# Kernel tuning notes

Measured on AMD Instinct MI355X. Metric: run time of the kernel, lower is better.

## Reference

```python
import jax, jax.numpy as jnp
import numpy as np

NUM_HEADS = 4  # nn.MultiheadAttention(num_heads=4)


def setup_inputs() -> dict:
    key = jax.random.key(0)
    ks = jax.random.split(key, 9)
    E, D, B, S = 16, 128, 8, 512
    H2 = D // 2
    s = 0.05
    return {
        "lstm_features": jax.random.normal(ks[0], (B, S, D), dtype=jnp.float32),
        "Wqkv": jax.random.normal(ks[1], (E, 3 * D, D), dtype=jnp.float32) * s,
        "bqkv": jax.random.normal(ks[2], (E, 3 * D), dtype=jnp.float32) * s,
        "Wo": jax.random.normal(ks[3], (E, D, D), dtype=jnp.float32) * s,
        "bo": jax.random.normal(ks[4], (E, D), dtype=jnp.float32) * s,
        "W1": jax.random.normal(ks[5], (E, H2, D), dtype=jnp.float32) * s,
        "b1": jax.random.normal(ks[6], (E, H2), dtype=jnp.float32) * s,
        "W2": jax.random.normal(ks[7], (E, 1, H2), dtype=jnp.float32) * s,
        "b2": jax.random.normal(ks[8], (E, 1), dtype=jnp.float32) * s,
    }


def reference(lstm_features, Wqkv, bqkv, Wo, bo, W1, b1, W2, b2):
    # lstm_features: [B, S, D]; params stacked over E=num_events.
    B, S, D = lstm_features.shape
    E = Wqkv.shape[0]
    H = NUM_HEADS
    Dh = D // H

    # Grouped in-projection for all events at once: [E, B, S, 3D]
    qkv = jnp.einsum("bsd,ekd->ebsk", lstm_features, Wqkv) + bqkv[:, None, None, :]
    q, k, v = jnp.split(qkv, 3, axis=-1)  # each [E, B, S, D]

    def heads(t):  # [E,B,S,D] -> [E,B,H,S,Dh]
        return t.reshape(E, B, S, H, Dh).transpose(0, 1, 3, 2, 4)

    q, k, v = heads(q), heads(k), heads(v)

    scale = 1.0 / jnp.sqrt(jnp.asarray(Dh, dtype=lstm_features.dtype))
    scores = jnp.einsum("ebhqd,ebhkd->ebhqk", q, k) * scale  # [E,B,H,S,S]
    attn = jax.nn.softmax(scores, axis=-1)
    ctx = jnp.einsum("ebhqk,ebhkd->ebhqd", attn, v)  # [E,B,H,S,Dh]
    ctx = ctx.transpose(0, 1, 3, 2, 4).reshape(E, B, S, D)

    attended = jnp.einsum("ebsd,eod->ebso", ctx, Wo) + bo[:, None, None, :]

    # Per-event MLP head: D -> D//2 -> 1 (dropout is identity in eval)
    h = jax.nn.relu(jnp.einsum("ebsd,ehd->ebsh", attended, W1) + b1[:, None, None, :])
    logits = jnp.einsum("ebsh,eoh->ebso", h, W2) + b2[:, None, None, :]  # [E,B,S,1]
    logits = logits[..., 0]  # [E,B,S]

    # torch.stack(..., dim=2) -> [B, S, E]
    return logits.transpose(1, 2, 0)
```

## Files before the change

### kernel.cpp

```cpp
#include <hip/hip_runtime.h>


#define E_ 16
#define B_ 8
#define S_ 512
#define D_ 128
#define H_ 4
#define DH_ 32
#define H2_ 64
#define M_ (B_ * S_)
#define QK_SCALE 0.17677669529663687f

typedef __attribute__((ext_vector_type(4))) short bf16x4;
typedef __attribute__((ext_vector_type(8))) short bf16x8;
typedef __attribute__((ext_vector_type(4))) float f32x4;

__device__ __forceinline__ short f2bf(float f) {
    unsigned u = __builtin_bit_cast(unsigned, f);
    u += 0x7fffu + ((u >> 16) & 1u);
    return (short)(u >> 16);
}

__device__ __forceinline__ bf16x8 cat8(bf16x4 lo, bf16x4 hi) {
    return __builtin_shufflevector(lo, hi, 0, 1, 2, 3, 4, 5, 6, 7);
}

__global__ __launch_bounds__(256) void convert_kernel(
    const float* __restrict__ x, const float* __restrict__ w,
    const float* __restrict__ wo, const float* __restrict__ w1,
    short* __restrict__ xbf, short* __restrict__ wbf,
    short* __restrict__ wobf, short* __restrict__ w1bf)
{
    const int XN  = (M_ * D_) / 8;
    const int WN  = (E_ * 3 * D_ * D_) / 8;
    const int WON = (E_ * D_ * D_) / 8;
    const int W1N = (E_ * H2_ * D_) / 8;
    int idx = blockIdx.x * 256 + threadIdx.x;
    const float* src; short* dst; int off;
    if (idx < XN)                        { src = x;  dst = xbf;  off = idx; }
    else if (idx < XN + WN)              { src = w;  dst = wbf;  off = idx - XN; }
    else if (idx < XN + WN + WON)        { src = wo; dst = wobf; off = idx - XN - WN; }
    else if (idx < XN + WN + WON + W1N)  { src = w1; dst = w1bf; off = idx - XN - WN - WON; }
    else return;
    float4 v0 = *(const float4*)&src[(size_t)off * 8];
    float4 v1 = *(const float4*)&src[(size_t)off * 8 + 4];
    bf16x8 o;
    o[0] = f2bf(v0.x); o[1] = f2bf(v0.y); o[2] = f2bf(v0.z); o[3] = f2bf(v0.w);
    o[4] = f2bf(v1.x); o[5] = f2bf(v1.y); o[6] = f2bf(v1.z); o[7] = f2bf(v1.w);
    *(bf16x8*)&dst[(size_t)off * 8] = o;
}

__global__ __launch_bounds__(256) void qkv_mfma_kernel(
    const short* __restrict__ xbf,
    const short* __restrict__ wbf,
    const float* __restrict__ bqkv,
    short* __restrict__ q, short* __restrict__ k, short* __restrict__ v)
{
    __shared__ __align__(16) char lds[2 * 64 * 136 * 2];
    short (*xs)[136] = (short(*)[136])lds;
    short (*ws)[136] = (short(*)[136])(lds + 64 * 136 * 2);

    const int ct = blockIdx.x;
    const int rt = blockIdx.y;
    const int e  = blockIdx.z;
    const int tid = threadIdx.x;
    const int w    = tid >> 6;
    const int lane = tid & 63;
    const int l15  = lane & 15;
    const int g    = lane >> 4;

    #pragma unroll
    for (int p = 0; p < 4; ++p) {
        int idx = tid + p * 256;
        int row = idx >> 4, c8 = (idx & 15) * 8;
        *(bf16x8*)&xs[row][c8] =
            *(const bf16x8*)&xbf[(size_t)(rt * 64 + row) * 128 + c8];
        *(bf16x8*)&ws[row][c8] =
            *(const bf16x8*)&wbf[((size_t)e * 384 + ct * 64 + row) * 128 + c8];
    }
    __syncthreads();

    const int n0 = (w & 1) * 32;
    const int m0 = (w >> 1) * 32;
    f32x4 acc00 = {0.f,0.f,0.f,0.f}, acc01 = {0.f,0.f,0.f,0.f};
    f32x4 acc10 = {0.f,0.f,0.f,0.f}, acc11 = {0.f,0.f,0.f,0.f};

    #pragma unroll
    for (int kk = 0; kk < 128; kk += 32) {
        bf16x8 A0 = cat8(*(const bf16x4*)&ws[n0      + l15][kk + 4 * g],
                         *(const bf16x4*)&ws[n0      + l15][kk + 16 + 4 * g]);
        bf16x8 A1 = cat8(*(const bf16x4*)&ws[n0 + 16 + l15][kk + 4 * g],
                         *(const bf16x4*)&ws[n0 + 16 + l15][kk + 16 + 4 * g]);
        bf16x8 B0 = cat8(*(const bf16x4*)&xs[m0      + l15][kk + 4 * g],
                         *(const bf16x4*)&xs[m0      + l15][kk + 16 + 4 * g]);
        bf16x8 B1 = cat8(*(const bf16x4*)&xs[m0 + 16 + l15][kk + 4 * g],
                         *(const bf16x4*)&xs[m0 + 16 + l15][kk + 16 + 4 * g]);
        acc00 = __builtin_amdgcn_mfma_f32_16x16x32_bf16(A0, B0, acc00, 0, 0, 0);
        acc01 = __builtin_amdgcn_mfma_f32_16x16x32_bf16(A0, B1, acc01, 0, 0, 0);
        acc10 = __builtin_amdgcn_mfma_f32_16x16x32_bf16(A1, B0, acc10, 0, 0, 0);
        acc11 = __builtin_amdgcn_mfma_f32_16x16x32_bf16(A1, B1, acc11, 0, 0, 0);
    }

    if (ct < 4) {
        short* dst = (ct < 2) ? q : k;
        const float scale = (ct < 2) ? QK_SCALE : 1.0f;
        #define STORE_QK(ACC, NS, MS) {                                          \
            const int jb = ct * 64 + n0 + (NS) * 16 + 4 * g;                     \
            const int d  = jb & 127;                                             \
            const int h  = d >> 5, dh = d & 31;                                  \
            const float b0 = bqkv[e * 384 + jb + 0];                             \
            const float b1 = bqkv[e * 384 + jb + 1];                             \
            const float b2 = bqkv[e * 384 + jb + 2];                             \
            const float b3 = bqkv[e * 384 + jb + 3];                             \
            const int m  = rt * 64 + m0 + (MS) * 16 + l15;                       \
            const int bb = m >> 9, s = m & 511;                                  \
            bf16x4 o;                                                            \
            o[0] = f2bf((ACC[0] + b0) * scale);                                  \
            o[1] = f2bf((ACC[1] + b1) * scale);                                  \
            o[2] = f2bf((ACC[2] + b2) * scale);                                  \
            o[3] = f2bf((ACC[3] + b3) * scale);                                  \
            *(bf16x4*)&dst[((((size_t)e * B_ + bb) * H_ + h) * S_ + s) * DH_ + dh] = o; \
        }
        STORE_QK(acc00, 0, 0); STORE_QK(acc01, 0, 1);
        STORE_QK(acc10, 1, 0); STORE_QK(acc11, 1, 1);
        #undef STORE_QK
    } else {
        __syncthreads();
        float (*rp)[68] = (float(*)[68])lds;
        #define RP(ACC, NS, MS) {                                                \
            const int jl = n0 + (NS) * 16 + 4 * g;                               \
            const int ml = m0 + (MS) * 16 + l15;                                 \
            rp[jl + 0][ml] = ACC[0]; rp[jl + 1][ml] = ACC[1];                    \
            rp[jl + 2][ml] = ACC[2]; rp[jl + 3][ml] = ACC[3];                    \
        }
        RP(acc00, 0, 0); RP(acc01, 0, 1); RP(acc10, 1, 0); RP(acc11, 1, 1);
        #undef RP
        __syncthreads();
        const int bb = (rt * 64) >> 9;
        const int sb = (rt * 64) & 511;
        #pragma unroll
        for (int p = 0; p < 2; ++p) {
            int task = tid + p * 256;
            int jl = task >> 3, sc = (task & 7) * 8;
            const int col = ct * 64 + jl;
            const int d = col & 127, h = d >> 5, dh = d & 31;
            const float bias = bqkv[e * 384 + col];
            bf16x8 o;
            #pragma unroll
            for (int j = 0; j < 8; ++j) o[j] = f2bf(rp[jl][sc + j] + bias);
            *(bf16x8*)&v[((((size_t)e * B_ + bb) * H_ + h) * DH_ + dh) * S_ + sb + sc] = o;
        }
    }
}

__global__ __launch_bounds__(512) void attn_kernel(
    const short* __restrict__ q, const short* __restrict__ k,
    const short* __restrict__ vt, short* __restrict__ ctxbf)
{
    __shared__ alignas(16) short Ks[256][40];
    __shared__ alignas(16) short VTs[32][520];

    const int bh  = blockIdx.x;
    const int e   = blockIdx.y;
    const int tid = threadIdx.x;
    const int w    = tid >> 6;
    const int lane = tid & 63;
    const int l15  = lane & 15;
    const int g    = lane >> 4;

    const size_t base = ((size_t)e * 32 + bh) * (S_ * DH_);
    const short* qg = q  + base;
    const short* kg = k  + base;
    const short* vg = vt + base;

    {
        int d = tid >> 4, c0 = (tid & 15) * 32;
        const uint4* src = (const uint4*)(vg + (size_t)d * S_ + c0);
        uint4* dst = (uint4*)((char*)&VTs[0][0] + (size_t)d * 1040 + c0 * 2);
        dst[0] = src[0]; dst[1] = src[1]; dst[2] = src[2]; dst[3] = src[3];
    }
    {
        int row = tid >> 1, ch = (tid & 1) * 16;
        const uint4* src = (const uint4*)(kg + (size_t)row * DH_ + ch);
        uint4* dst = (uint4*)((char*)&Ks[0][0] + (size_t)row * 80 + ch * 2);
        dst[0] = src[0]; dst[1] = src[1];
    }
    bf16x8 bq[4];
    int qrow[4];
    #pragma unroll
    for (int qf = 0; qf < 4; ++qf) {
        qrow[qf] = w * 64 + qf * 16 + l15;
        bf16x4 lo = *(const bf16x4*)(qg + (size_t)qrow[qf] * DH_ + 4 * g);
        bf16x4 hi = *(const bf16x4*)(qg + (size_t)qrow[qf] * DH_ + 16 + 4 * g);
        bq[qf] = cat8(lo, hi);
    }
    __syncthreads();

    f32x4 acc0[4] = {}, acc1[4] = {};
    float lsum[4] = {0.f, 0.f, 0.f, 0.f};

    for (int half = 0; half < 2; ++half) {
        for (int kt = 0; kt < 8; ++kt) {
            bf16x8 ka[2];
            #pragma unroll
            for (int tt = 0; tt < 2; ++tt) {
                const int row_l = (kt * 2 + tt) * 16 + l15;
                const char* kp = (const char*)&Ks[0][0] + (size_t)row_l * 80 + g * 8;
                ka[tt] = cat8(*(const bf16x4*)kp, *(const bf16x4*)(kp + 32));
            }
            const int keyb = half * 256 + kt * 32;
            const char* vp = (const char*)&VTs[0][0] + (size_t)l15 * 1040 + (keyb + 4 * g) * 2;
            bf16x8 va0 = cat8(*(const bf16x4*)vp, *(const bf16x4*)(vp + 32));
            const char* vp1 = vp + 16 * 1040;
            bf16x8 va1 = cat8(*(const bf16x4*)vp1, *(const bf16x4*)(vp1 + 32));

            #pragma unroll
            for (int qf = 0; qf < 4; ++qf) {
                f32x4 z = {0.f, 0.f, 0.f, 0.f};
                f32x4 s0 = __builtin_amdgcn_mfma_f32_16x16x32_bf16(ka[0], bq[qf], z, 0, 0, 0);
                f32x4 s1 = __builtin_amdgcn_mfma_f32_16x16x32_bf16(ka[1], bq[qf], z, 0, 0, 0);
                float p0 = __expf(s0[0]), p1 = __expf(s0[1]);
                float p2 = __expf(s0[2]), p3 = __expf(s0[3]);
                float p4 = __expf(s1[0]), p5 = __expf(s1[1]);
                float p6 = __expf(s1[2]), p7 = __expf(s1[3]);
                lsum[qf] += ((p0 + p1) + (p2 + p3)) + ((p4 + p5) + (p6 + p7));
                bf16x8 pf;
                pf[0] = f2bf(p0); pf[1] = f2bf(p1); pf[2] = f2bf(p2); pf[3] = f2bf(p3);
                pf[4] = f2bf(p4); pf[5] = f2bf(p5); pf[6] = f2bf(p6); pf[7] = f2bf(p7);
                acc0[qf] = __builtin_amdgcn_mfma_f32_16x16x32_bf16(va0, pf, acc0[qf], 0, 0, 0);
                acc1[qf] = __builtin_amdgcn_mfma_f32_16x16x32_bf16(va1, pf, acc1[qf], 0, 0, 0);
            }
        }
        if (half == 0) {
            __syncthreads();
            int row = tid >> 1, ch = (tid & 1) * 16;
            const uint4* src = (const uint4*)(kg + (size_t)(256 + row) * DH_ + ch);
            uint4* dst = (uint4*)((char*)&Ks[0][0] + (size_t)row * 80 + ch * 2);
            dst[0] = src[0]; dst[1] = src[1];
            __syncthreads();
        }
    }

    const int b = bh >> 2, h = bh & 3;
    #pragma unroll
    for (int qf = 0; qf < 4; ++qf) {
        float ls = lsum[qf];
        ls += __shfl_xor(ls, 16);
        ls += __shfl_xor(ls, 32);
        const float inv = 1.0f / ls;
        short* cg = ctxbf + (((size_t)(e * B_ + b) * S_ + qrow[qf]) * D_ + h * DH_);
        bf16x4 o0, o1;
        #pragma unroll
        for (int r = 0; r < 4; ++r) {
            o0[r] = f2bf(acc0[qf][r] * inv);
            o1[r] = f2bf(acc1[qf][r] * inv);
        }
        *(bf16x4*)&cg[4 * g]      = o0;
        *(bf16x4*)&cg[16 + 4 * g] = o1;
    }
}

__global__ __launch_bounds__(256) void head_mfma_kernel(
    const short* __restrict__ ctxbf,
    const short* __restrict__ wobf,
    const float* __restrict__ bo,
    const short* __restrict__ w1bf,
    const float* __restrict__ b1,
    const float* __restrict__ W2,
    const float* __restrict__ b2,
    float* __restrict__ out)
{
    __shared__ alignas(16) short Wos[128][136];
    __shared__ alignas(16) short cts[64][136];

    const int mt  = blockIdx.x;
    const int e   = blockIdx.y;
    const int tid = threadIdx.x;
    const int w    = tid >> 6;
    const int lane = tid & 63;
    const int l15  = lane & 15;
    const int g    = lane >> 4;

    #pragma unroll
    for (int p = 0; p < 8; ++p) {
        int idx = tid + p * 256;
        int row = idx >> 4, c8 = (idx & 15) * 8;
        *(bf16x8*)&Wos[row][c8] =
            *(const bf16x8*)&wobf[((size_t)e * 128 + row) * 128 + c8];
    }
    #pragma unroll
    for (int p = 0; p < 4; ++p) {
        int idx = tid + p * 256;
        int row = idx >> 4, c8 = (idx & 15) * 8;
        *(bf16x8*)&cts[row][c8] =
            *(const bf16x8*)&ctxbf[((size_t)e * M_ + mt * 64 + row) * 128 + c8];
    }
    __syncthreads();

    f32x4 accA[8] = {};
    #pragma unroll
    for (int kk = 0; kk < 128; kk += 32) {
        bf16x8 a = cat8(*(const bf16x4*)&cts[w * 16 + l15][kk + 4 * g],
                        *(const bf16x4*)&cts[w * 16 + l15][kk + 16 + 4 * g]);
        #pragma unroll
        for (int t = 0; t < 8; ++t) {
            bf16x8 bfr = cat8(*(const bf16x4*)&Wos[t * 16 + l15][kk + 4 * g],
                              *(const bf16x4*)&Wos[t * 16 + l15][kk + 16 + 4 * g]);
            accA[t] = __builtin_amdgcn_mfma_f32_16x16x32_bf16(a, bfr, accA[t], 0, 0, 0);
        }
    }
    __syncthreads();

    #pragma unroll
    for (int p = 0; p < 4; ++p) {
        int idx = tid + p * 256;
        int row = idx >> 4, c8 = (idx & 15) * 8;
        *(bf16x8*)&Wos[row][c8] =
            *(const bf16x8*)&w1bf[((size_t)e * 64 + row) * 128 + c8];
    }
    #pragma unroll
    for (int t = 0; t < 8; ++t) {
        const float bov = bo[e * 128 + t * 16 + l15];
        #pragma unroll
        for (int r = 0; r < 4; ++r)
            cts[w * 16 + 4 * g + r][t * 16 + l15] = f2bf(accA[t][r] + bov);
    }
    __syncthreads();

    f32x4 accB[4] = {};
    #pragma unroll
    for (int kk = 0; kk < 128; kk += 32) {
        bf16x8 a = cat8(*(const bf16x4*)&cts[w * 16 + l15][kk + 4 * g],
                        *(const bf16x4*)&cts[w * 16 + l15][kk + 16 + 4 * g]);
        #pragma unroll
        for (int t = 0; t < 4; ++t) {
            bf16x8 bfr = cat8(*(const bf16x4*)&Wos[t * 16 + l15][kk + 4 * g],
                              *(const bf16x4*)&Wos[t * 16 + l15][kk + 16 + 4 * g]);
            accB[t] = __builtin_amdgcn_mfma_f32_16x16x32_bf16(a, bfr, accB[t], 0, 0, 0);
        }
    }

    float b1v[4], w2v[4];
    #pragma unroll
    for (int t = 0; t < 4; ++t) {
        b1v[t] = b1[e * 64 + t * 16 + l15];
        w2v[t] = W2[e * 64 + t * 16 + l15];
    }
    const float b2v = b2[e];
    #pragma unroll
    for (int r = 0; r < 4; ++r) {
        float s = 0.f;
        #pragma unroll
        for (int t = 0; t < 4; ++t)
            s += fmaxf(accB[t][r] + b1v[t], 0.f) * w2v[t];
        s += __shfl_xor(s, 1);
        s += __shfl_xor(s, 2);
        s += __shfl_xor(s, 4);
        s += __shfl_xor(s, 8);
        if (l15 == 0) {
            const int m = mt * 64 + w * 16 + 4 * g + r;
            const int bb = m >> 9, ss = m & 511;
            out[((size_t)(bb * S_ + ss)) * E_ + e] = s + b2v;
        }
    }
}

extern "C" void kernel_launch(void* const* d_in, const int* in_sizes, int n_in,
                              void* d_out, int out_size, void* d_ws, size_t ws_size,
                              hipStream_t stream) {
    const float* x    = (const float*)d_in[0];
    const float* Wqkv = (const float*)d_in[1];
    const float* bqkv = (const float*)d_in[2];
    const float* Wo   = (const float*)d_in[3];
    const float* bo   = (const float*)d_in[4];
    const float* W1   = (const float*)d_in[5];
    const float* b1   = (const float*)d_in[6];
    const float* W2   = (const float*)d_in[7];
    const float* b2   = (const float*)d_in[8];
    float* out = (float*)d_out;

    const size_t SZ = (size_t)E_ * B_ * H_ * S_ * DH_;
    short* qb    = (short*)d_ws;
    short* kb    = qb + SZ;
    short* vtb   = kb + SZ;
    short* ctxbf = vtb + SZ;
    short* xbf   = ctxbf + SZ;
    short* wbf   = xbf + (size_t)M_ * D_;
    short* wobf  = wbf + (size_t)E_ * 3 * D_ * D_;
    short* w1bf  = wobf + (size_t)E_ * D_ * D_;

    convert_kernel<<<dim3(832), 256, 0, stream>>>(x, Wqkv, Wo, W1, xbf, wbf, wobf, w1bf);
    qkv_mfma_kernel<<<dim3(6, 64, 16), 256, 0, stream>>>(xbf, wbf, bqkv, qb, kb, vtb);
    attn_kernel<<<dim3(32, 16), 512, 0, stream>>>(qb, kb, vtb, ctxbf);
    head_mfma_kernel<<<dim3(64, 16), 256, 0, stream>>>(ctxbf, wobf, bo, w1bf, b1, W2, b2, out);
}
```

Measured before the change: 79.41 us.

## Fuse fp32-to-bf16 conversion into GEMM loads and use exp2 softmax

Removes the separate conversion kernel by having the QKV and head GEMM kernels load fp32 inputs and weights directly and pack them to bf16 while staging into LDS. This saves one kernel launch and a write-then-read round trip through the bf16 workspace. It also folds log2(e) into the Q scale so the softmax can use the hardware exp2 instruction, switches to the library bf16 conversion, and partially unrolls the attention key loop. The cost is that weights are now read and converted redundantly by many blocks, and twice as many bytes are loaded per tile.

New measurement: 85.32 us. 7.4% more time.

```diff
diff --git a/kernel.cpp b/kernel.cpp
--- a/kernel.cpp
+++ b/kernel.cpp
@@ -1,4 +1,5 @@
 #include <hip/hip_runtime.h>
+#include <hip/hip_bf16.h>
 
 
 #define E_ 16
@@ -9,50 +10,29 @@
 #define DH_ 32
 #define H2_ 64
 #define M_ (B_ * S_)
-#define QK_SCALE 0.17677669529663687f
+#define QK_SCALE_L2E 0.25503472437616588f
 
 typedef __attribute__((ext_vector_type(4))) short bf16x4;
 typedef __attribute__((ext_vector_type(8))) short bf16x8;
 typedef __attribute__((ext_vector_type(4))) float f32x4;
 
-__device__ __forceinline__ short f2bf(float f) {
-    unsigned u = __builtin_bit_cast(unsigned, f);
-    u += 0x7fffu + ((u >> 16) & 1u);
-    return (short)(u >> 16);
+__device__ __forceinline__ short f2b(float f) {
+    return __builtin_bit_cast(short, __float2bfloat16(f));
+}
+
+__device__ __forceinline__ bf16x4 pack4(float4 v) {
+    bf16x4 o;
+    o[0] = f2b(v.x); o[1] = f2b(v.y); o[2] = f2b(v.z); o[3] = f2b(v.w);
+    return o;
 }
 
 __device__ __forceinline__ bf16x8 cat8(bf16x4 lo, bf16x4 hi) {
     return __builtin_shufflevector(lo, hi, 0, 1, 2, 3, 4, 5, 6, 7);
 }
 
-__global__ __launch_bounds__(256) void convert_kernel(
-    const float* __restrict__ x, const float* __restrict__ w,
-    const float* __restrict__ wo, const float* __restrict__ w1,
-    short* __restrict__ xbf, short* __restrict__ wbf,
-    short* __restrict__ wobf, short* __restrict__ w1bf)
-{
-    const int XN  = (M_ * D_) / 8;
-    const int WN  = (E_ * 3 * D_ * D_) / 8;
-    const int WON = (E_ * D_ * D_) / 8;
-    const int W1N = (E_ * H2_ * D_) / 8;
-    int idx = blockIdx.x * 256 + threadIdx.x;
-    const float* src; short* dst; int off;
-    if (idx < XN)                        { src = x;  dst = xbf;  off = idx; }
-    else if (idx < XN + WN)              { src = w;  dst = wbf;  off = idx - XN; }
-    else if (idx < XN + WN + WON)        { src = wo; dst = wobf; off = idx - XN - WN; }
-    else if (idx < XN + WN + WON + W1N)  { src = w1; dst = w1bf; off = idx - XN - WN - WON; }
-    else return;
-    float4 v0 = *(const float4*)&src[(size_t)off * 8];
-    float4 v1 = *(const float4*)&src[(size_t)off * 8 + 4];
-    bf16x8 o;
-    o[0] = f2bf(v0.x); o[1] = f2bf(v0.y); o[2] = f2bf(v0.z); o[3] = f2bf(v0.w);
-    o[4] = f2bf(v1.x); o[5] = f2bf(v1.y); o[6] = f2bf(v1.z); o[7] = f2bf(v1.w);
-    *(bf16x8*)&dst[(size_t)off * 8] = o;
-}
-
 __global__ __launch_bounds__(256) void qkv_mfma_kernel(
-    const short* __restrict__ xbf,
-    const short* __restrict__ wbf,
+    const float* __restrict__ x,
+    const float* __restrict__ Wqkv,
     const float* __restrict__ bqkv,
     short* __restrict__ q, short* __restrict__ k, short* __restrict__ v)
 {
@@ -70,13 +50,13 @@
     const int g    = lane >> 4;
 
     #pragma unroll
-    for (int p = 0; p < 4; ++p) {
+    for (int p = 0; p < 8; ++p) {
         int idx = tid + p * 256;
-        int row = idx >> 4, c8 = (idx & 15) * 8;
-        *(bf16x8*)&xs[row][c8] =
-            *(const bf16x8*)&xbf[(size_t)(rt * 64 + row) * 128 + c8];
-        *(bf16x8*)&ws[row][c8] =
-            *(const bf16x8*)&wbf[((size_t)e * 384 + ct * 64 + row) * 128 + c8];
+        int row = idx >> 5, c4 = (idx & 31) * 4;
+        *(bf16x4*)&xs[row][c4] =
+            pack4(*(const float4*)&x[(size_t)(rt * 64 + row) * 128 + c4]);
+        *(bf16x4*)&ws[row][c4] =
+            pack4(*(const float4*)&Wqkv[((size_t)e * 384 + ct * 64 + row) * 128 + c4]);
     }
     __syncthreads();
 
@@ -103,7 +83,7 @@
 
     if (ct < 4) {
         short* dst = (ct < 2) ? q : k;
-        const float scale = (ct < 2) ? QK_SCALE : 1.0f;
+        const float scale = (ct < 2) ? QK_SCALE_L2E : 1.0f;
         #define STORE_QK(ACC, NS, MS) {                                          \
             const int jb = ct * 64 + n0 + (NS) * 16 + 4 * g;                     \
             const int d  = jb & 127;                                             \
@@ -115,10 +95,10 @@
             const int m  = rt * 64 + m0 + (MS) * 16 + l15;                       \
             const int bb = m >> 9, s = m & 511;                                  \
             bf16x4 o;                                                            \
-            o[0] = f2bf((ACC[0] + b0) * scale);                                  \
-            o[1] = f2bf((ACC[1] + b1) * scale);                                  \
-            o[2] = f2bf((ACC[2] + b2) * scale);                                  \
-            o[3] = f2bf((ACC[3] + b3) * scale);                                  \
+            o[0] = f2b((ACC[0] + b0) * scale);                                   \
+            o[1] = f2b((ACC[1] + b1) * scale);                                   \
+            o[2] = f2b((ACC[2] + b2) * scale);                                   \
+            o[3] = f2b((ACC[3] + b3) * scale);                                   \
             *(bf16x4*)&dst[((((size_t)e * B_ + bb) * H_ + h) * S_ + s) * DH_ + dh] = o; \
         }
         STORE_QK(acc00, 0, 0); STORE_QK(acc01, 0, 1);
@@ -147,7 +127,7 @@
             const float bias = bqkv[e * 384 + col];
             bf16x8 o;
             #pragma unroll
-            for (int j = 0; j < 8; ++j) o[j] = f2bf(rp[jl][sc + j] + bias);
+            for (int j = 0; j < 8; ++j) o[j] = f2b(rp[jl][sc + j] + bias);
             *(bf16x8*)&v[((((size_t)e * B_ + bb) * H_ + h) * DH_ + dh) * S_ + sb + sc] = o;
         }
     }
@@ -200,6 +180,7 @@
     float lsum[4] = {0.f, 0.f, 0.f, 0.f};
 
     for (int half = 0; half < 2; ++half) {
+        #pragma unroll 2
         for (int kt = 0; kt < 8; ++kt) {
             bf16x8 ka[2];
             #pragma unroll
@@ -219,14 +200,18 @@
                 f32x4 z = {0.f, 0.f, 0.f, 0.f};
                 f32x4 s0 = __builtin_amdgcn_mfma_f32_16x16x32_bf16(ka[0], bq[qf], z, 0, 0, 0);
                 f32x4 s1 = __builtin_amdgcn_mfma_f32_16x16x32_bf16(ka[1], bq[qf], z, 0, 0, 0);
-                float p0 = __expf(s0[0]), p1 = __expf(s0[1]);
-                float p2 = __expf(s0[2]), p3 = __expf(s0[3]);
-                float p4 = __expf(s1[0]), p5 = __expf(s1[1]);
-                float p6 = __expf(s1[2]), p7 = __expf(s1[3]);
+                float p0 = __builtin_amdgcn_exp2f(s0[0]);
+                float p1 = __builtin_amdgcn_exp2f(s0[1]);
+                float p2 = __builtin_amdgcn_exp2f(s0[2]);
+                float p3 = __builtin_amdgcn_exp2f(s0[3]);
+                float p4 = __builtin_amdgcn_exp2f(s1[0]);
+                float p5 = __builtin_amdgcn_exp2f(s1[1]);
+                float p6 = __builtin_amdgcn_exp2f(s1[2]);
+                float p7 = __builtin_amdgcn_exp2f(s1[3]);
                 lsum[qf] += ((p0 + p1) + (p2 + p3)) + ((p4 + p5) + (p6 + p7));
                 bf16x8 pf;
-                pf[0] = f2bf(p0); pf[1] = f2bf(p1); pf[2] = f2bf(p2); pf[3] = f2bf(p3);
-                pf[4] = f2bf(p4); pf[5] = f2bf(p5); pf[6] = f2bf(p6); pf[7] = f2bf(p7);
+                pf[0] = f2b(p0); pf[1] = f2b(p1); pf[2] = f2b(p2); pf[3] = f2b(p3);
+                pf[4] = f2b(p4); pf[5] = f2b(p5); pf[6] = f2b(p6); pf[7] = f2b(p7);
                 acc0[qf] = __builtin_amdgcn_mfma_f32_16x16x32_bf16(va0, pf, acc0[qf], 0, 0, 0);
                 acc1[qf] = __builtin_amdgcn_mfma_f32_16x16x32_bf16(va1, pf, acc1[qf], 0, 0, 0);
             }
@@ -252,8 +237,8 @@
         bf16x4 o0, o1;
         #pragma unroll
         for (int r = 0; r < 4; ++r) {
-            o0[r] = f2bf(acc0[qf][r] * inv);
-            o1[r] = f2bf(acc1[qf][r] * inv);
+            o0[r] = f2b(acc0[qf][r] * inv);
+            o1[r] = f2b(acc1[qf][r] * inv);
         }
         *(bf16x4*)&cg[4 * g]      = o0;
         *(bf16x4*)&cg[16 + 4 * g] = o1;
@@ -262,9 +247,9 @@
 
 __global__ __launch_bounds__(256) void head_mfma_kernel(
     const short* __restrict__ ctxbf,
-    const short* __restrict__ wobf,
+    const float* __restrict__ Wo,
     const float* __restrict__ bo,
-    const short* __restrict__ w1bf,
+    const float* __restrict__ W1,
     const float* __restrict__ b1,
     const float* __restrict__ W2,
     const float* __restrict__ b2,
@@ -282,11 +267,11 @@
     const int g    = lane >> 4;
 
     #pragma unroll
-    for (int p = 0; p < 8; ++p) {
+    for (int p = 0; p < 16; ++p) {
         int idx = tid + p * 256;
-        int row = idx >> 4, c8 = (idx & 15) * 8;
-        *(bf16x8*)&Wos[row][c8] =
-            *(const bf16x8*)&wobf[((size_t)e * 128 + row) * 128 + c8];
+        int row = idx >> 5, c4 = (idx & 31) * 4;
+        *(bf16x4*)&Wos[row][c4] =
+            pack4(*(const float4*)&Wo[((size_t)e * 128 + row) * 128 + c4]);
     }
     #pragma unroll
     for (int p = 0; p < 4; ++p) {
@@ -312,18 +297,18 @@
     __syncthreads();
 
     #pragma unroll
-    for (int p = 0; p < 4; ++p) {
+    for (int p = 0; p < 8; ++p) {
         int idx = tid + p * 256;
-        int row = idx >> 4, c8 = (idx & 15) * 8;
-        *(bf16x8*)&Wos[row][c8] =
-            *(const bf16x8*)&w1bf[((size_t)e * 64 + row) * 128 + c8];
+        int row = idx >> 5, c4 = (idx & 31) * 4;
+        *(bf16x4*)&Wos[row][c4] =
+            pack4(*(const float4*)&W1[((size_t)e * 64 + row) * 128 + c4]);
     }
     #pragma unroll
     for (int t = 0; t < 8; ++t) {
         const float bov = bo[e * 128 + t * 16 + l15];
         #pragma unroll
         for (int r = 0; r < 4; ++r)
-            cts[w * 16 + 4 * g + r][t * 16 + l15] = f2bf(accA[t][r] + bov);
+            cts[w * 16 + 4 * g + r][t * 16 + l15] = f2b(accA[t][r] + bov);
     }
     __syncthreads();
 
@@ -384,13 +369,8 @@
     short* kb    = qb + SZ;
     short* vtb   = kb + SZ;
     short* ctxbf = vtb + SZ;
-    short* xbf   = ctxbf + SZ;
-    short* wbf   = xbf + (size_t)M_ * D_;
-    short* wobf  = wbf + (size_t)E_ * 3 * D_ * D_;
-    short* w1bf  = wobf + (size_t)E_ * D_ * D_;
-
-    convert_kernel<<<dim3(832), 256, 0, stream>>>(x, Wqkv, Wo, W1, xbf, wbf, wobf, w1bf);
-    qkv_mfma_kernel<<<dim3(6, 64, 16), 256, 0, stream>>>(xbf, wbf, bqkv, qb, kb, vtb);
+
+    qkv_mfma_kernel<<<dim3(6, 64, 16), 256, 0, stream>>>(x, Wqkv, bqkv, qb, kb, vtb);
     attn_kernel<<<dim3(32, 16), 512, 0, stream>>>(qb, kb, vtb, ctxbf);
-    head_mfma_kernel<<<dim3(64, 16), 256, 0, stream>>>(ctxbf, wobf, bo, w1bf, b1, W2, b2, out);
-}
+    head_mfma_kernel<<<dim3(64, 16), 256, 0, stream>>>(ctxbf, Wo, bo, W1, b1, W2, b2, out);
+}
```
